# Optimization experiments

Measured on AMD Instinct MI355X. Metric: run time of the kernel, lower is better.

## Reference

```python
import jax, jax.numpy as jnp
import numpy as np

K = 3; STRIDE = 1; PAD = 1
IN_C = 256; OUT_C = 512
M = 5; TABLE_SIZE = 16
D = K * K * IN_C  # 2304


def _P(v, m):
    # ALSH preprocessing transform: append norm powers ||v||^2, ||v||^4, ...
    n2 = jnp.sum(v * v)
    powers = jnp.stack([n2 ** (2 ** i) for i in range(m)])
    return jnp.concatenate([v, powers])


def _Q(v, m):
    # ALSH query transform: append m halves
    return jnp.concatenate([v, jnp.full((m,), 0.5, v.dtype)])


def _hash_index(a, v):
    # hf followed by fmod(table_size).abs() as in the torch module
    h = jnp.floor(jnp.dot(a, v))
    return jnp.abs(jnp.mod(h, TABLE_SIZE)).astype(jnp.int32)


def _im2col(x):
    # x: (N, C, H, W) -> (K*K*C, N*h2*w2), rows ordered (kh, kw, c) to match
    # the (out, k, k, in) kernel flattening of the original module.
    N, C, H, W = x.shape
    h2 = (H - K + 2 * PAD) // STRIDE + 1
    w2 = (W - K + 2 * PAD) // STRIDE + 1
    xp = jnp.pad(x, ((0, 0), (0, 0), (PAD, PAD), (PAD, PAD)))
    cols = []
    for i in range(K):          # small fixed loop (k*k = 9)
        for j in range(K):
            cols.append(xp[:, :, i:i + h2 * STRIDE:STRIDE, j:j + w2 * STRIDE:STRIDE])
    p = jnp.stack(cols, 0)                 # (K*K, N, C, h2, w2)
    p = p.transpose(0, 2, 1, 3, 4)         # (K*K, C, N, h2, w2)
    return p.reshape(K * K * C, N * h2 * w2), h2, w2


def setup_inputs() -> dict:
    key = jax.random.key(0)
    k1, k2, k3, k4 = jax.random.split(key, 4)
    stdv = 1.0 / np.sqrt(IN_C * K * K)
    x = jax.random.normal(k1, (16, IN_C, 56, 56), dtype=jnp.float32)
    kernels = jax.random.uniform(k2, (OUT_C, D), dtype=jnp.float32,
                                 minval=-stdv, maxval=stdv)
    bias = jax.random.uniform(k3, (1, OUT_C, 1, 1), dtype=jnp.float32,
                              minval=-stdv, maxval=stdv)
    a = jax.random.normal(k4, (D + M,), dtype=jnp.float32)
    return {"x": x, "kernels": kernels, "bias": bias, "a": a, "mode": 0}


def reference(x, kernels, bias, a, mode):
    N = x.shape[0]
    patch_matr, h2, w2 = _im2col(x)  # (D, N*h2*w2)

    # --- build ALSH table: hash index per kernel row (non-differentiable) ---
    kernel_idx = jax.lax.stop_gradient(
        jax.vmap(lambda kr: _hash_index(a, _P(kr, M)))(kernels))  # (OUT_C,)

    # --- query: max over each patch row, normalized to unit vector ---
    max_row = patch_matr.max(axis=1)                    # (D,)
    unit = max_row / jnp.linalg.norm(max_row)
    q_idx = jax.lax.stop_gradient(_hash_index(a, _Q(unit, M)))

    # --- routed subset matmul, expressed as a row mask (jit-safe) ---
    mask = (kernel_idx == q_idx)                        # (OUT_C,) bool
    count = mask.sum()
    full = kernels @ patch_matr                         # (OUT_C, N*h2*w2)
    scale = jnp.where(count > 0, count / OUT_C, 1.0).astype(full.dtype)
    out = jnp.where(count > 0,
                    jnp.where(mask[:, None], full, 0.0) / scale,
                    full)

    out = out.reshape(OUT_C, N, h2 * w2).transpose(1, 0, 2)
    out = out.reshape(N, OUT_C, h2, w2)
    return out + bias
```

## Files before the change

### kernel.cpp

```cpp
#include <hip/hip_runtime.h>
#include <math.h>

#define IN_C   256
#define OUT_C  512
#define HW     3136
#define W_     56
#define D_     2304
#define TBL    16


#define XB_OFF 2375680ULL
#define XB_ROW 1856
#define P_OFF  7483392

typedef __attribute__((ext_vector_type(8))) __bf16 bf16x8;
typedef __attribute__((ext_vector_type(4))) float f32x4;

__device__ __forceinline__ ushort f2bf(float f) {
  uint b = __float_as_uint(f);
  b = b + 0x7FFFu + ((b >> 16) & 1u);
  return (ushort)(b >> 16);
}


__global__ __launch_bounds__(256) void k_setup(const float* __restrict__ x,
                                               const float* __restrict__ kern,
                                               const float* __restrict__ a,
                                               float* __restrict__ ws) {
  __shared__ __align__(16) float smem[64 * 57];
  int bx = blockIdx.x, t = threadIdx.x;

  if (bx < 3712) {
    int c0i = bx & 3;
    int n = (bx >> 2) & 15;
    int yp = bx >> 6;
    int c0 = c0i * 64, cgbase = c0i * 2;
    ushort* xb = (ushort*)((char*)ws + XB_OFF);
    const size_t CGS = (size_t)16 * 58 * XB_ROW;
    size_t rb0 = (size_t)(n * 58 + yp) * XB_ROW;
    uint4 z4 = make_uint4(0u, 0u, 0u, 0u);

    if (yp == 0 || yp == 57) {
      for (int e = t; e < 464; e += 256) {
        int cg_l = e / 232, k = e - cg_l * 232;
        *(uint4*)&xb[rb0 + (size_t)(cgbase + cg_l) * CGS + (size_t)k * 8] = z4;
      }
      return;
    }
    if (t < 16) {
      int cg_l = t >> 3, r = t & 7;
      int wp = (r >> 2) ? 57 : 0, oct = r & 3;
      *(uint4*)&xb[rb0 + (size_t)(cgbase + cg_l) * CGS + wp * 32 + oct * 8] = z4;
    }
    int y = yp - 1;
    float* Lf = smem;
    for (int e = t; e < 3584; e += 256) {
      int ci = e / 56, w = e - ci * 56;
      Lf[ci * 57 + w] = x[(size_t)(n * 256 + c0 + ci) * 3136 + y * 56 + w];
    }
    __syncthreads();
    for (int e = t; e < 448; e += 256) {
      int w = e >> 3, cg_l = (e >> 2) & 1, oct = e & 3;
      int cb = cg_l * 32 + oct * 8;
      uint pk[4];
#pragma unroll
      for (int k = 0; k < 4; k++) {
        uint lo = f2bf(Lf[(cb + 2 * k) * 57 + w]);
        uint hi = f2bf(Lf[(cb + 2 * k + 1) * 57 + w]);
        pk[k] = lo | (hi << 16);
      }
      *(uint4*)&xb[rb0 + (size_t)(cgbase + cg_l) * CGS + (w + 1) * 32 + oct * 8] =
          make_uint4(pk[0], pk[1], pk[2], pk[3]);
    }
  } else if (bx < 4736) {
    int idx = bx - 3712;
    int c = idx & 255, part = idx >> 8;
    float m[3][3];
#pragma unroll
    for (int i = 0; i < 3; i++)
#pragma unroll
      for (int j = 0; j < 3; j++) m[i][j] = -INFINITY;
    for (int e = t; e < 4 * HW; e += 256) {
      int nl = e / HW;
      int rem = e - nl * HW;
      int r = rem / W_;
      int s = rem - r * W_;
      float v = x[(size_t)((part * 4 + nl) * IN_C + c) * HW + rem];
      bool rc[3] = { r <= 54, true, r >= 1 };
      bool sc[3] = { s <= 54, true, s >= 1 };
#pragma unroll
      for (int i = 0; i < 3; i++)
#pragma unroll
        for (int j = 0; j < 3; j++)
          if (rc[i] && sc[j]) m[i][j] = fmaxf(m[i][j], v);
    }
#pragma unroll
    for (int i = 0; i < 3; i++)
#pragma unroll
      for (int j = 0; j < 3; j++)
        for (int o = 32; o; o >>= 1)
          m[i][j] = fmaxf(m[i][j], __shfl_down(m[i][j], o, 64));
    float* red = smem;
    int lane = t & 63, wid = t >> 6;
    if (lane == 0) {
#pragma unroll
      for (int i = 0; i < 3; i++)
#pragma unroll
        for (int j = 0; j < 3; j++) red[wid * 9 + i * 3 + j] = m[i][j];
    }
    __syncthreads();
    if (t < 9) {
      float v = fmaxf(fmaxf(red[0 * 9 + t], red[1 * 9 + t]),
                      fmaxf(red[2 * 9 + t], red[3 * 9 + t]));
      ws[P_OFF + (size_t)part * 2304 + (size_t)t * IN_C + c] = v;
    }
  } else {
    int o = bx - 4736;
    const float* kr = kern + (size_t)o * D_;
    double sd = 0, sn = 0;
    for (int d = t; d < D_; d += 256) {
      double w = (double)kr[d];
      sd += (double)a[d] * w;
      sn += w * w;
    }
    double* sh = (double*)smem;
    double* sh2 = sh + 8;
    int lane = t & 63, wid = t >> 6;
    for (int off = 32; off; off >>= 1) {
      sd += __shfl_down(sd, off, 64);
      sn += __shfl_down(sn, off, 64);
    }
    if (lane == 0) { sh[wid] = sd; sh2[wid] = sn; }
    __syncthreads();
    if (t == 0) {
      double td = 0, tn = 0;
      for (int w = 0; w < 4; w++) { td += sh[w]; tn += sh2[w]; }
      double p1 = tn, p2 = p1 * p1, p4 = p2 * p2, p8 = p4 * p4, p16 = p8 * p8;
      td += (double)a[D_] * p1 + (double)a[D_ + 1] * p2 + (double)a[D_ + 2] * p4 +
            (double)a[D_ + 3] * p8 + (double)a[D_ + 4] * p16;
      long long h = (long long)floor(td);
      ((int*)ws)[2304 + o] = (int)((h % TBL + TBL) % TBL);
    }
  }
}

__global__ __launch_bounds__(512) void k_route(const float* __restrict__ a,
                                               float* __restrict__ ws) {
  int t = threadIdx.x;
  const float* P = ws + P_OFF;
  __shared__ double sh[8], sh2[8];
  __shared__ int shq, c1, c2;
  double sd = 0.0, sq = 0.0;
  if (t < 256) {
    for (int d = t; d < D_; d += 256) {
      float v = fmaxf(fmaxf(P[d], P[2304 + d]), fmaxf(P[4608 + d], P[6912 + d]));
      if ((d >> 8) != 4) v = fmaxf(v, 0.0f);
      double dv = (double)v;
      sd += (double)a[d] * dv;
      sq += dv * dv;
    }
    for (int o = 32; o; o >>= 1) {
      sd += __shfl_down(sd, o, 64);
      sq += __shfl_down(sq, o, 64);
    }
    if ((t & 63) == 0) { sh[t >> 6] = sd; sh2[t >> 6] = sq; }
  }
  __syncthreads();
  if (t == 0) {
    double td = 0, tq = 0;
    for (int w = 0; w < 4; w++) { td += sh[w]; tq += sh2[w]; }
    double dot = td / sqrt(tq);
    dot += 0.5 * ((double)a[D_] + (double)a[D_ + 1] + (double)a[D_ + 2] +
                  (double)a[D_ + 3] + (double)a[D_ + 4]);
    long long h = (long long)floor(dot);
    int q = (int)((h % TBL + TBL) % TBL);
    ((int*)ws)[2816] = q;
    shq = q;
    c1 = 0; c2 = 0;
  }
  __syncthreads();
  int* hashk = (int*)ws + 2304;
  int* cntp = (int*)ws + 2817;
  float* scalep = ws + 2818;
  int* active = (int*)ws + 2819;
  int* inact = (int*)ws + 3331;
  int q = shq;
  bool m = (hashk[t] == q);
  if (m) active[atomicAdd(&c1, 1)] = t;
  else   inact[atomicAdd(&c2, 1)] = t;
  __syncthreads();
  int c = c1;
  if (c == 0) active[t] = t;
  if (t == 0) {
    if (c > 0) { *cntp = c; *scalep = 512.0f / (float)c; }
    else       { *cntp = 512; *scalep = 1.0f; }
  }
}

__global__ __launch_bounds__(256) void k_prep(const float* __restrict__ kern,
                                              float* __restrict__ ws) {
  const int* iws = (const int*)ws;
  int cnt = iws[2817];
  const int* active = iws + 2819;
  uint* Wc = (uint*)((char*)ws + 16384);
  int s = blockIdx.x, t = threadIdx.x;
  if (s < cnt) {
    int oc = active[s];
    const float* src = kern + (size_t)oc * D_;
    for (int e = t; e < 1152; e += 256) {
      uint lo = f2bf(src[2 * e]);
      uint hi = f2bf(src[2 * e + 1]);
      Wc[(size_t)s * 1152 + e] = lo | (hi << 16);
    }
  } else {
    for (int e = t; e < 1152; e += 256) Wc[(size_t)s * 1152 + e] = 0;
  }
}

#define XSTR 40
#define ASTR 40
#define XSTRIDE 40
#define ASTRIDE 104

__global__ __launch_bounds__(256, 2) void k_convx(const float* __restrict__ bias,
                                                  const float* __restrict__ ws,
                                                  float* __restrict__ out) {
  const int* iws = (const int*)ws;
  int cnt = iws[2817];
  int octile = blockIdx.y;
  int rt = blockIdx.x;
  int n = blockIdx.z;
  int t = threadIdx.x;

  {
    int base = octile * 128;
    int lo = base < cnt ? cnt : base;
    int hi = base + 128;
    if (lo < hi) {
      const int* inact = iws + 3331;
      size_t nbase = (size_t)n * OUT_C * HW;
      int nin = hi - lo;
      for (int e = t; e < nin * 56; e += 256) {
        int j = e / 56, f = e - j * 56;
        int oc = inact[lo - cnt + j];
        float bv = bias[oc];
        ((float4*)out)[(nbase + (size_t)oc * HW + rt * 224) / 4 + f] =
            make_float4(bv, bv, bv, bv);
      }
    }
    if (base >= cnt) return;
  }

  float sc = ws[2818];
  const int* active = iws + 2819;
  const ushort* Wc = (const ushort*)((const char*)ws + 16384);
  const ushort* xb = (const ushort*)((const char*)ws + XB_OFF);

  int lane = t & 63, wid = t >> 6;
  int quad = lane >> 4, l16 = lane & 15;
  int ochalf = wid & 1, pxhalf = wid >> 1;

  __shared__ __align__(16) ushort X_lds[2][348 * XSTR];
  __shared__ __align__(16) ushort A_lds[2][128 * ASTR];

  int pbase[7];
#pragma unroll
  for (int b = 0; b < 7; b++) {
    int pxl = pxhalf * 112 + b * 16 + l16;
    int rl = pxl / 56;
    int col = pxl - rl * 56;
    pbase[b] = ((rl + 1) * 58 + (col + 1)) * XSTR;
  }

  int ar0 = t >> 2;
  int aq = (t & 3) * 8;
  const ushort* Wrow0 = Wc + (size_t)(octile * 128 + ar0) * D_ + aq;
  const ushort* Wrow1 = Wrow0 + (size_t)64 * D_;
  int aoff0 = ar0 * ASTR + aq;
  int aoff1 = (ar0 + 64) * ASTR + aq;

  const size_t CGS = (size_t)16 * 58 * XB_ROW;
  const ushort* xsrc = xb + (size_t)(n * 58 + rt * 4) * XB_ROW;

  f32x4 acc[4][7];
#pragma unroll
  for (int a = 0; a < 4; a++)
#pragma unroll
    for (int b = 0; b < 7; b++) acc[a][b] = (f32x4){0.f, 0.f, 0.f, 0.f};

  uint4 pA0, pA1, nA0, nA1;
  uint4 xh; int xhj = 0; bool xhv = false;

  {
    uint4 a0 = *(const uint4*)(Wrow0);
    uint4 a1 = *(const uint4*)(Wrow1);
    *(uint4*)&A_lds[0][aoff0] = a0;
    *(uint4*)&A_lds[0][aoff1] = a1;
    for (int j = t; j < 1392; j += 256)
      *(uint4*)&X_lds[0][(j >> 2) * XSTR + (j & 3) * 8] =
          *(const uint4*)(xsrc + (size_t)j * 8);
    pA0 = *(const uint4*)(Wrow0 + 256);
    pA1 = *(const uint4*)(Wrow1 + 256);
  }
  __syncthreads();

  for (int cc = 0; cc < 8; ++cc) {
    const int xc = cc & 1;
#pragma unroll
    for (int tap = 0; tap < 9; ++tap) {
      const int cur = (cc + tap) & 1;
      const bool last = (cc == 7) && (tap == 8);
      const int tap2 = (tap + 2) % 9;
      const int cc2 = cc + (tap + 2) / 9;
      if (cc2 < 8) {
        int goff = tap2 * 256 + cc2 * 32;
        nA0 = *(const uint4*)(Wrow0 + goff);
        nA1 = *(const uint4*)(Wrow1 + goff);
      }
      const bool xpf = (tap < 6) && (cc < 7) && (t < 232);
      uint4 xv; int xj = tap * 232 + t;
      if (xpf)
        xv = *(const uint4*)(xsrc + (size_t)(cc + 1) * CGS + (size_t)xj * 8);

      const int kh = tap / 3, kw = tap - kh * 3;
      const int poff = ((kh - 1) * 58 + (kw - 1)) * XSTR + quad * 8;
      bf16x8 af[4];
#pragma unroll
      for (int a = 0; a < 4; a++) {
        union { uint4 u; bf16x8 v; } cv;
        cv.u = *(const uint4*)&A_lds[cur][(ochalf * 64 + a * 16 + l16) * ASTR +
                                          quad * 8];
        af[a] = cv.v;
      }
      __builtin_amdgcn_s_setprio(1);
#pragma unroll
      for (int b = 0; b < 7; b++) {
        union { uint4 u; bf16x8 v; } cv;
        cv.u = *(const uint4*)&X_lds[xc][pbase[b] + poff];
        bf16x8 xf = cv.v;
#pragma unroll
        for (int a = 0; a < 4; a++)
          acc[a][b] = __builtin_amdgcn_mfma_f32_16x16x32_bf16(af[a], xf,
                                                              acc[a][b], 0, 0, 0);
      }
      __builtin_amdgcn_s_setprio(0);

      if (!last) {
        *(uint4*)&A_lds[cur ^ 1][aoff0] = pA0;
        *(uint4*)&A_lds[cur ^ 1][aoff1] = pA1;
      }
      if (xhv)
        *(uint4*)&X_lds[xc ^ 1][(xhj >> 2) * XSTR + (xhj & 3) * 8] = xh;
      __syncthreads();
      pA0 = nA0; pA1 = nA1;
      xh = xv; xhj = xj; xhv = xpf;
    }
  }

  size_t nbase = (size_t)n * OUT_C * HW;
#pragma unroll
  for (int a = 0; a < 4; a++) {
#pragma unroll
    for (int r = 0; r < 4; r++) {
      int slot = octile * 128 + ochalf * 64 + a * 16 + quad * 4 + r;
      if (slot < cnt) {
        int oc = active[slot];
        float bv = bias[oc];
        size_t obase = nbase + (size_t)oc * HW + rt * 224 + pxhalf * 112 + l16;
#pragma unroll
        for (int b = 0; b < 7; b++)
          out[obase + b * 16] = acc[a][b][r] * sc + bv;
      }
    }
  }
}


__global__ __launch_bounds__(256) void k_chanmax(const float* __restrict__ x,
                                                 float* __restrict__ ws) {
  int c = blockIdx.x, t = threadIdx.x;
  float m[3][3];
#pragma unroll
  for (int i = 0; i < 3; i++)
#pragma unroll
    for (int j = 0; j < 3; j++) m[i][j] = -INFINITY;
  for (int e = t; e < 16 * HW; e += 256) {
    int n = e / HW;
    int rem = e - n * HW;
    int r = rem / W_;
    int s = rem - r * W_;
    float v = x[(size_t)(n * IN_C + c) * HW + rem];
    bool rc[3] = { r <= 54, true, r >= 1 };
    bool sc[3] = { s <= 54, true, s >= 1 };
#pragma unroll
    for (int i = 0; i < 3; i++)
#pragma unroll
      for (int j = 0; j < 3; j++)
        if (rc[i] && sc[j]) m[i][j] = fmaxf(m[i][j], v);
  }
#pragma unroll
  for (int i = 0; i < 3; i++)
#pragma unroll
    for (int j = 0; j < 3; j++)
      for (int o = 32; o; o >>= 1)
        m[i][j] = fmaxf(m[i][j], __shfl_down(m[i][j], o, 64));
  __shared__ float red[4][9];
  int lane = t & 63, wid = t >> 6;
  if (lane == 0) {
#pragma unroll
    for (int i = 0; i < 3; i++)
#pragma unroll
      for (int j = 0; j < 3; j++) red[wid][i * 3 + j] = m[i][j];
  }
  __syncthreads();
  if (t < 9) {
    float v = fmaxf(fmaxf(red[0][t], red[1][t]), fmaxf(red[2][t], red[3][t]));
    int i = t / 3, j = t - i * 3;
    if (i != 1 || j != 1) v = fmaxf(v, 0.0f);
    ws[(size_t)t * IN_C + c] = v;
  }
}

__global__ __launch_bounds__(256) void k_qhash(const float* __restrict__ a,
                                               float* __restrict__ ws) {
  const float* max_row = ws;
  int t = threadIdx.x;
  double sd = 0.0, sq = 0.0;
  for (int d = t; d < D_; d += 256) {
    double v = (double)max_row[d];
    sd += (double)a[d] * v;
    sq += v * v;
  }
  __shared__ double sh[8], sh2[8];
  int lane = t & 63, wid = t >> 6;
  for (int o = 32; o; o >>= 1) {
    sd += __shfl_down(sd, o, 64);
    sq += __shfl_down(sq, o, 64);
  }
  if (lane == 0) { sh[wid] = sd; sh2[wid] = sq; }
  __syncthreads();
  if (t == 0) {
    double td = 0, tq = 0;
    for (int w = 0; w < 4; w++) { td += sh[w]; tq += sh2[w]; }
    double dot = td / sqrt(tq);
    dot += 0.5 * ((double)a[D_] + (double)a[D_ + 1] + (double)a[D_ + 2] +
                  (double)a[D_ + 3] + (double)a[D_ + 4]);
    long long h = (long long)floor(dot);
    ((int*)ws)[2816] = (int)((h % TBL + TBL) % TBL);
  }
}

__global__ __launch_bounds__(256) void k_khash(const float* __restrict__ kern,
                                               const float* __restrict__ a,
                                               float* __restrict__ ws) {
  int o = blockIdx.x, t = threadIdx.x;
  const float* kr = kern + (size_t)o * D_;
  double sd = 0, sn = 0;
  for (int d = t; d < D_; d += 256) {
    double w = (double)kr[d];
    sd += (double)a[d] * w;
    sn += w * w;
  }
  __shared__ double sh[8], sh2[8];
  int lane = t & 63, wid = t >> 6;
  for (int off = 32; off; off >>= 1) {
    sd += __shfl_down(sd, off, 64);
    sn += __shfl_down(sn, off, 64);
  }
  if (lane == 0) { sh[wid] = sd; sh2[wid] = sn; }
  __syncthreads();
  if (t == 0) {
    double td = 0, tn = 0;
    for (int w = 0; w < 4; w++) { td += sh[w]; tn += sh2[w]; }
    double p1 = tn, p2 = p1 * p1, p4 = p2 * p2, p8 = p4 * p4, p16 = p8 * p8;
    td += (double)a[D_] * p1 + (double)a[D_ + 1] * p2 + (double)a[D_ + 2] * p4 +
          (double)a[D_ + 3] * p8 + (double)a[D_ + 4] * p16;
    long long h = (long long)floor(td);
    ((int*)ws)[2304 + o] = (int)((h % TBL + TBL) % TBL);
  }
}

__global__ __launch_bounds__(512) void k_select(float* __restrict__ ws) {
  int t = threadIdx.x;
  int* hashk = (int*)ws + 2304;
  int* qidx = (int*)ws + 2816;
  int* cntp = (int*)ws + 2817;
  float* scalep = ws + 2818;
  int* active = (int*)ws + 2819;
  int* flags = (int*)ws + 3331;
  __shared__ int cnt;
  if (t == 0) cnt = 0;
  active[t] = 0;
  __syncthreads();
  int q = *qidx;
  bool m = (hashk[t] == q);
  if (m) {
    int p = atomicAdd(&cnt, 1);
    active[p] = t;
  }
  __syncthreads();
  int c = cnt;
  flags[t] = (c == 0) ? 1 : (m ? 1 : 0);
  if (c == 0) active[t] = t;
  if (t == 0) {
    if (c > 0) { *cntp = c; *scalep = 512.0f / (float)c; }
    else       { *cntp = 512; *scalep = 1.0f; }
  }
}

__global__ __launch_bounds__(256) void k_biasfill(const float* __restrict__ bias,
                                                  const float* __restrict__ ws,
                                                  float* __restrict__ out) {
  const int* flags = (const int*)ws + 3331;
  const int total4 = 16 * OUT_C * HW / 4;
  int stride = gridDim.x * blockDim.x;
  for (int i = blockIdx.x * blockDim.x + threadIdx.x; i < total4; i += stride) {
    int o = (i / 784) & (OUT_C - 1);
    if (!flags[o]) {
      float b = bias[o];
      ((float4*)out)[i] = make_float4(b, b, b, b);
    }
  }
}

__global__ __launch_bounds__(256, 2) void k_conv(const float* __restrict__ x,
                                                 const float* __restrict__ bias,
                                                 const float* __restrict__ ws,
                                                 float* __restrict__ out) {
  const int* iws = (const int*)ws;
  int cnt = iws[2817];
  int octile = blockIdx.y;
  if (octile * 128 >= cnt) return;
  float sc = ws[2818];
  const int* active = iws + 2819;
  const ushort* Wc = (const ushort*)((const char*)ws + 16384);
  int rt = blockIdx.x;
  int n = blockIdx.z;
  int t = threadIdx.x;
  int lane = t & 63, wid = t >> 6;
  int quad = lane >> 4, l16 = lane & 15;
  int ochalf = wid & 1, pxhalf = wid >> 1;
  __shared__ __align__(16) ushort X_lds[348 * XSTRIDE];
  __shared__ __align__(16) ushort A_lds[128 * ASTRIDE];
  const float* xin = x + (size_t)n * IN_C * HW;
  int pbase[7];
#pragma unroll
  for (int b = 0; b < 7; b++) {
    int pxl = pxhalf * 112 + b * 16 + l16;
    int rl = pxl / 56;
    int col = pxl - rl * 56;
    pbase[b] = ((rl + 1) * 58 + (col + 1)) * XSTRIDE;
  }
  f32x4 acc[4][7];
#pragma unroll
  for (int a = 0; a < 4; a++)
#pragma unroll
    for (int b = 0; b < 7; b++) acc[a][b] = (f32x4){0.f, 0.f, 0.f, 0.f};
  for (int cc = 0; cc < 8; ++cc) {
    int c0 = cc * 32;
    __syncthreads();
    for (int e = t; e < 1392; e += 256) {
      int q = e / 348;
      int p = e - q * 348;
      int rl = p / 58;
      int cp = p - rl * 58;
      int y = rt * 4 - 1 + rl;
      int xx = cp - 1;
      float vv[8];
      if ((unsigned)y < 56u && (unsigned)xx < 56u) {
        const float* src = xin + (size_t)(c0 + q * 8) * HW + y * W_ + xx;
#pragma unroll
        for (int k = 0; k < 8; k++) vv[k] = src[(size_t)k * HW];
      } else {
#pragma unroll
        for (int k = 0; k < 8; k++) vv[k] = 0.f;
      }
      uint4 pk;
      pk.x = (uint)f2bf(vv[0]) | ((uint)f2bf(vv[1]) << 16);
      pk.y = (uint)f2bf(vv[2]) | ((uint)f2bf(vv[3]) << 16);
      pk.z = (uint)f2bf(vv[4]) | ((uint)f2bf(vv[5]) << 16);
      pk.w = (uint)f2bf(vv[6]) | ((uint)f2bf(vv[7]) << 16);
      *(uint4*)&X_lds[p * XSTRIDE + q * 8] = pk;
    }
    for (int kh = 0; kh < 3; ++kh) {
      __syncthreads();
      for (int e = t; e < 1536; e += 256) {
        int oc = e / 12;
        int seg = e - oc * 12;
        int tl = seg >> 2, q = seg & 3;
        uint4 v = *(const uint4*)(Wc + (size_t)(octile * 128 + oc) * D_ +
                                  (kh * 3 + tl) * IN_C + c0 + q * 8);
        *(uint4*)&A_lds[oc * ASTRIDE + tl * 32 + q * 8] = v;
      }
      __syncthreads();
      int di = kh - 1;
#pragma unroll
      for (int djj = 0; djj < 3; ++djj) {
        int poff = (di * 58 + (djj - 1)) * XSTRIDE + quad * 8;
        bf16x8 bfr[7];
#pragma unroll
        for (int b = 0; b < 7; b++) {
          union { uint4 u; bf16x8 v; } cv;
          cv.u = *(const uint4*)&X_lds[pbase[b] + poff];
          bfr[b] = cv.v;
        }
#pragma unroll
        for (int a = 0; a < 4; a++) {
          union { uint4 u; bf16x8 v; } cv;
          cv.u = *(const uint4*)&A_lds[(ochalf * 64 + a * 16 + l16) * ASTRIDE +
                                       djj * 32 + quad * 8];
          bf16x8 af = cv.v;
#pragma unroll
          for (int b = 0; b < 7; b++)
            acc[a][b] = __builtin_amdgcn_mfma_f32_16x16x32_bf16(af, bfr[b],
                                                                acc[a][b], 0, 0, 0);
        }
      }
    }
  }
  size_t nbase = (size_t)n * OUT_C * HW;
#pragma unroll
  for (int a = 0; a < 4; a++) {
#pragma unroll
    for (int r = 0; r < 4; r++) {
      int slot = octile * 128 + ochalf * 64 + a * 16 + quad * 4 + r;
      if (slot < cnt) {
        int oc = active[slot];
        float bv = bias[oc];
        size_t obase = nbase + (size_t)oc * HW + rt * 224 + pxhalf * 112 + l16;
#pragma unroll
        for (int b = 0; b < 7; b++)
          out[obase + b * 16] = acc[a][b][r] * sc + bv;
      }
    }
  }
}

extern "C" void kernel_launch(void* const* d_in, const int* in_sizes, int n_in,
                              void* d_out, int out_size, void* d_ws, size_t ws_size,
                              hipStream_t stream) {
  const float* x    = (const float*)d_in[0];
  const float* kern = (const float*)d_in[1];
  const float* bias = (const float*)d_in[2];
  const float* a    = (const float*)d_in[3];
  float* out = (float*)d_out;
  float* ws  = (float*)d_ws;

  const size_t need = 29933568ULL + 4 * 2304 * 4;

  if (ws_size >= need) {
    k_setup<<<dim3(5248), dim3(256), 0, stream>>>(x, kern, a, ws);
    k_route<<<dim3(1), dim3(512), 0, stream>>>(a, ws);
    k_prep<<<dim3(OUT_C), dim3(256), 0, stream>>>(kern, ws);
    k_convx<<<dim3(14, 4, 16), dim3(256), 0, stream>>>(bias, ws, out);
  } else {
    k_chanmax<<<dim3(IN_C), dim3(256), 0, stream>>>(x, ws);
    k_qhash<<<dim3(1), dim3(256), 0, stream>>>(a, ws);
    k_khash<<<dim3(OUT_C), dim3(256), 0, stream>>>(kern, a, ws);
    k_select<<<dim3(1), dim3(512), 0, stream>>>(ws);
    k_prep<<<dim3(OUT_C), dim3(256), 0, stream>>>(kern, ws);
    k_biasfill<<<dim3(4096), dim3(256), 0, stream>>>(bias, ws, out);
    k_conv<<<dim3(14, 4, 16), dim3(256), 0, stream>>>(x, bias, ws, out);
  }
}
```

Measured before the change: 298.6 us.

## Load weight fragments straight to registers and fold bf16 conversion into setup

```diff
diff --git a/kernel.cpp b/kernel.cpp
--- a/kernel.cpp
+++ b/kernel.cpp
@@ -114,7 +114,7 @@
                       fmaxf(red[2 * 9 + t], red[3 * 9 + t]));
       ws[P_OFF + (size_t)part * 2304 + (size_t)t * IN_C + c] = v;
     }
-  } else {
+  } else if (bx < 5248) {
     int o = bx - 4736;
     const float* kr = kern + (size_t)o * D_;
     double sd = 0, sn = 0;
@@ -140,6 +140,15 @@
             (double)a[D_ + 3] * p8 + (double)a[D_ + 4] * p16;
       long long h = (long long)floor(td);
       ((int*)ws)[2304 + o] = (int)((h % TBL + TBL) % TBL);
+    }
+  } else {
+    int s = bx - 5248;
+    uint* Wc = (uint*)((char*)ws + 16384);
+    const float* src = kern + (size_t)s * D_;
+    for (int e = t; e < 1152; e += 256) {
+      uint lo = f2bf(src[2 * e]);
+      uint hi = f2bf(src[2 * e + 1]);
+      Wc[(size_t)s * 1152 + e] = lo | (hi << 16);
     }
   }
 }
@@ -197,28 +206,7 @@
   }
 }
 
-__global__ __launch_bounds__(256) void k_prep(const float* __restrict__ kern,
-                                              float* __restrict__ ws) {
-  const int* iws = (const int*)ws;
-  int cnt = iws[2817];
-  const int* active = iws + 2819;
-  uint* Wc = (uint*)((char*)ws + 16384);
-  int s = blockIdx.x, t = threadIdx.x;
-  if (s < cnt) {
-    int oc = active[s];
-    const float* src = kern + (size_t)oc * D_;
-    for (int e = t; e < 1152; e += 256) {
-      uint lo = f2bf(src[2 * e]);
-      uint hi = f2bf(src[2 * e + 1]);
-      Wc[(size_t)s * 1152 + e] = lo | (hi << 16);
-    }
-  } else {
-    for (int e = t; e < 1152; e += 256) Wc[(size_t)s * 1152 + e] = 0;
-  }
-}
-
 #define XSTR 40
-#define ASTR 40
 #define XSTRIDE 40
 #define ASTRIDE 104
 
@@ -253,7 +241,7 @@
 
   float sc = ws[2818];
   const int* active = iws + 2819;
-  const ushort* Wc = (const ushort*)((const char*)ws + 16384);
+  const char* Wcb = (const char*)ws + 16384;
   const ushort* xb = (const ushort*)((const char*)ws + XB_OFF);
 
   int lane = t & 63, wid = t >> 6;
@@ -261,7 +249,6 @@
   int ochalf = wid & 1, pxhalf = wid >> 1;
 
   __shared__ __align__(16) ushort X_lds[2][348 * XSTR];
-  __shared__ __align__(16) ushort A_lds[2][128 * ASTR];
 
   int pbase[7];
 #pragma unroll
@@ -272,12 +259,13 @@
     pbase[b] = ((rl + 1) * 58 + (col + 1)) * XSTR;
   }
 
-  int ar0 = t >> 2;
-  int aq = (t & 3) * 8;
-  const ushort* Wrow0 = Wc + (size_t)(octile * 128 + ar0) * D_ + aq;
-  const ushort* Wrow1 = Wrow0 + (size_t)64 * D_;
-  int aoff0 = ar0 * ASTR + aq;
-  int aoff1 = (ar0 + 64) * ASTR + aq;
+  uint woff[4];
+#pragma unroll
+  for (int a = 0; a < 4; a++) {
+    int slot = octile * 128 + ochalf * 64 + a * 16 + l16;
+    int aoc = (slot < cnt) ? active[slot] : 0;
+    woff[a] = (uint)aoc * 4608u + (uint)quad * 16u;
+  }
 
   const size_t CGS = (size_t)16 * 58 * XB_ROW;
   const ushort* xsrc = xb + (size_t)(n * 58 + rt * 4) * XB_ROW;
@@ -288,19 +276,16 @@
 #pragma unroll
     for (int b = 0; b < 7; b++) acc[a][b] = (f32x4){0.f, 0.f, 0.f, 0.f};
 
-  uint4 pA0, pA1, nA0, nA1;
+  uint4 curA[4], nA[4];
   uint4 xh; int xhj = 0; bool xhv = false;
 
   {
-    uint4 a0 = *(const uint4*)(Wrow0);
-    uint4 a1 = *(const uint4*)(Wrow1);
-    *(uint4*)&A_lds[0][aoff0] = a0;
-    *(uint4*)&A_lds[0][aoff1] = a1;
+#pragma unroll
+    for (int a = 0; a < 4; a++)
+      curA[a] = *(const uint4*)(Wcb + woff[a]);
     for (int j = t; j < 1392; j += 256)
       *(uint4*)&X_lds[0][(j >> 2) * XSTR + (j & 3) * 8] =
           *(const uint4*)(xsrc + (size_t)j * 8);
-    pA0 = *(const uint4*)(Wrow0 + 256);
-    pA1 = *(const uint4*)(Wrow1 + 256);
   }
   __syncthreads();
 
@@ -308,14 +293,14 @@
     const int xc = cc & 1;
 #pragma unroll
     for (int tap = 0; tap < 9; ++tap) {
-      const int cur = (cc + tap) & 1;
-      const bool last = (cc == 7) && (tap == 8);
-      const int tap2 = (tap + 2) % 9;
-      const int cc2 = cc + (tap + 2) / 9;
-      if (cc2 < 8) {
-        int goff = tap2 * 256 + cc2 * 32;
-        nA0 = *(const uint4*)(Wrow0 + goff);
-        nA1 = *(const uint4*)(Wrow1 + goff);
+      const int tapn = (tap + 1) % 9;
+      const int ccn = cc + (tap + 1) / 9;
+      const bool havenext = !(cc == 7 && tap == 8);
+      if (havenext) {
+        uint go = (uint)(tapn * 512) + (uint)ccn * 64u;
+#pragma unroll
+        for (int a = 0; a < 4; a++)
+          nA[a] = *(const uint4*)(Wcb + woff[a] + go);
       }
       const bool xpf = (tap < 6) && (cc < 7) && (t < 232);
       uint4 xv; int xj = tap * 232 + t;
@@ -324,14 +309,6 @@
 
       const int kh = tap / 3, kw = tap - kh * 3;
       const int poff = ((kh - 1) * 58 + (kw - 1)) * XSTR + quad * 8;
-      bf16x8 af[4];
-#pragma unroll
-      for (int a = 0; a < 4; a++) {
-        union { uint4 u; bf16x8 v; } cv;
-        cv.u = *(const uint4*)&A_lds[cur][(ochalf * 64 + a * 16 + l16) * ASTR +
-                                          quad * 8];
-        af[a] = cv.v;
-      }
       __builtin_amdgcn_s_setprio(1);
 #pragma unroll
       for (int b = 0; b < 7; b++) {
@@ -339,22 +316,24 @@
         cv.u = *(const uint4*)&X_lds[xc][pbase[b] + poff];
         bf16x8 xf = cv.v;
 #pragma unroll
-        for (int a = 0; a < 4; a++)
-          acc[a][b] = __builtin_amdgcn_mfma_f32_16x16x32_bf16(af[a], xf,
+        for (int a = 0; a < 4; a++) {
+          union { uint4 u; bf16x8 v; } av;
+          av.u = curA[a];
+          acc[a][b] = __builtin_amdgcn_mfma_f32_16x16x32_bf16(av.v, xf,
                                                               acc[a][b], 0, 0, 0);
+        }
       }
       __builtin_amdgcn_s_setprio(0);
 
-      if (!last) {
-        *(uint4*)&A_lds[cur ^ 1][aoff0] = pA0;
-        *(uint4*)&A_lds[cur ^ 1][aoff1] = pA1;
-      }
       if (xhv)
         *(uint4*)&X_lds[xc ^ 1][(xhj >> 2) * XSTR + (xhj & 3) * 8] = xh;
-      __syncthreads();
-      pA0 = nA0; pA1 = nA1;
       xh = xv; xhj = xj; xhv = xpf;
-    }
+      if (havenext) {
+#pragma unroll
+        for (int a = 0; a < 4; a++) curA[a] = nA[a];
+      }
+    }
+    __syncthreads();
   }
 
   size_t nbase = (size_t)n * OUT_C * HW;
@@ -505,6 +484,22 @@
   if (t == 0) {
     if (c > 0) { *cntp = c; *scalep = 512.0f / (float)c; }
     else       { *cntp = 512; *scalep = 1.0f; }
+  }
+}
+
+__global__ __launch_bounds__(256) void k_prep(const float* __restrict__ kern,
+                                              float* __restrict__ ws) {
+  const int* iws = (const int*)ws;
+  int cnt = iws[2817];
+  const int* active = iws + 2819;
+  ushort* Wc = (ushort*)((char*)ws + 16384);
+  int s = blockIdx.x, t = threadIdx.x;
+  if (s < cnt) {
+    int oc = active[s];
+    const float* src = kern + (size_t)oc * D_;
+    for (int e = t; e < D_; e += 256) Wc[(size_t)s * D_ + e] = f2bf(src[e]);
+  } else {
+    for (int e = t; e < D_; e += 256) Wc[(size_t)s * D_ + e] = 0;
   }
 }
 
@@ -649,9 +644,8 @@
   const size_t need = 29933568ULL + 4 * 2304 * 4;
 
   if (ws_size >= need) {
-    k_setup<<<dim3(5248), dim3(256), 0, stream>>>(x, kern, a, ws);
+    k_setup<<<dim3(5760), dim3(256), 0, stream>>>(x, kern, a, ws);
     k_route<<<dim3(1), dim3(512), 0, stream>>>(a, ws);
-    k_prep<<<dim3(OUT_C), dim3(256), 0, stream>>>(kern, ws);
     k_convx<<<dim3(14, 4, 16), dim3(256), 0, stream>>>(bias, ws, out);
   } else {
     k_chanmax<<<dim3(IN_C), dim3(256), 0, stream>>>(x, ws);
```

Result: slower. 340.1 us (+13.9%).
